# Optimization experiments

Hardware: AMD Instinct MI355X
Metric: run time of the kernel (lower is better)

The kernel has to match this reference:

```python
import math
import jax, jax.numpy as jnp
import numpy as np

N_HEAD = 16
N_GROUPS = 32
EPS = 1e-05


def gelu(x):
    return 0.5 * x * (1.0 + jnp.tanh(math.sqrt(2.0 / math.pi) * (x + 0.044715 * x ** 3)))


def dp_group_norm(x, weight, bias, num_groups=N_GROUPS, eps=EPS):
    # x: [B, T, H]. torch F.group_norm on transposed [B, H, T] normalizes over
    # (channels_per_group, T) jointly per (batch, group).
    B, T, H = x.shape
    xg = x.reshape(B, T, num_groups, H // num_groups)
    mean = jnp.mean(xg, axis=(1, 3), keepdims=True)
    var = jnp.mean((xg - mean) ** 2, axis=(1, 3), keepdims=True)
    xn = ((xg - mean) / jnp.sqrt(var + eps)).reshape(B, T, H)
    return xn * weight + bias


def attention(x, w_attn, b_attn, w_aproj, b_aproj):
    B, T, H = x.shape
    hd = H // N_HEAD
    qkv = x @ w_attn + b_attn                      # [B, T, 3H]
    q, k, v = jnp.split(qkv, 3, axis=-1)
    q = q.reshape(B, T, N_HEAD, hd).transpose(0, 2, 1, 3)   # [B, nh, T, hd]
    k = k.reshape(B, T, N_HEAD, hd).transpose(0, 2, 1, 3)   # [B, nh, T, hd]
    v = v.reshape(B, T, N_HEAD, hd).transpose(0, 2, 1, 3)
    w = jnp.einsum('bhqd,bhkd->bhqk', q, k)        # no 1/sqrt(d): scale=False
    causal = jnp.tril(jnp.ones((T, T), dtype=x.dtype))
    w = w * causal - 1e10 * (1.0 - causal)
    w = jax.nn.softmax(w, axis=-1)
    a = jnp.einsum('bhqk,bhkd->bhqd', w, v)        # [B, nh, T, hd]
    a = a.transpose(0, 2, 1, 3).reshape(B, T, H)
    a = a @ w_aproj + b_aproj
    present = jnp.stack((k, v))                    # [2, B, nh, T, hd]
    return a, present


def setup_inputs() -> dict:
    key = jax.random.key(0)
    ks = jax.random.split(key, 6)
    B, T, H = 2, 2048, 1024
    return {
        'x': jax.random.normal(ks[0], (B, T, H), dtype=jnp.float32),
        'w_attn': jax.random.normal(ks[1], (H, 3 * H), dtype=jnp.float32) * 0.02,
        'b_attn': jnp.zeros((3 * H,), dtype=jnp.float32),
        'w_aproj': jax.random.normal(ks[2], (H, H), dtype=jnp.float32) * 0.02,
        'b_aproj': jnp.zeros((H,), dtype=jnp.float32),
        'ln1_w': jnp.ones((H,), dtype=jnp.float32),
        'ln1_b': jnp.zeros((H,), dtype=jnp.float32),
        'ln2_w': jnp.ones((H,), dtype=jnp.float32),
        'ln2_b': jnp.zeros((H,), dtype=jnp.float32),
        'w_fc': jax.random.normal(ks[3], (H, 4 * H), dtype=jnp.float32) * 0.02,
        'b_fc': jnp.zeros((4 * H,), dtype=jnp.float32),
        'w_mproj': jax.random.normal(ks[4], (4 * H, H), dtype=jnp.float32) * 0.02,
        'b_mproj': jnp.zeros((H,), dtype=jnp.float32),
    }


def reference(x, w_attn, b_attn, w_aproj, b_aproj, ln1_w, ln1_b, ln2_w, ln2_b,
              w_fc, b_fc, w_mproj, b_mproj):
    a, present = attention(dp_group_norm(x, ln1_w, ln1_b), w_attn, b_attn, w_aproj, b_aproj)
    x = x + a
    h = gelu(dp_group_norm(x, ln2_w, ln2_b) @ w_fc + b_fc)
    m = h @ w_mproj + b_mproj
    x = x + m
    return (x, present)
```

## Files before the change

### kernel.cpp

```cpp
#include <hip/hip_runtime.h>

#define B_  2
#define T_  2048
#define H_  1024
#define NH_ 16
#define HD_ 64
#define M_  (B_*T_)
#define AS_ 72

typedef __bf16 bf16x8 __attribute__((ext_vector_type(8)));
typedef float  floatx4 __attribute__((ext_vector_type(4)));

typedef __attribute__((address_space(1))) const unsigned int gas_u32;
typedef __attribute__((address_space(3))) unsigned int       las_u32;

__device__ __forceinline__ void gload_lds16(const __bf16* g, __bf16* l) {
    __builtin_amdgcn_global_load_lds((gas_u32*)g, (las_u32*)l, 16, 0, 0);
}

__global__ __launch_bounds__(256) void transpose_bf16(
    const float* __restrict__ in, __bf16* __restrict__ out, int K, int N)
{
    __shared__ float tile[32][33];
    const int k0 = blockIdx.x * 32, n0 = blockIdx.y * 32;
    const int tx = threadIdx.x & 31, ty = threadIdx.x >> 5;
#pragma unroll
    for (int i = 0; i < 32; i += 8)
        tile[ty + i][tx] = in[(size_t)(k0 + ty + i) * N + (n0 + tx)];
    __syncthreads();
#pragma unroll
    for (int i = 0; i < 32; i += 8)
        out[(size_t)(n0 + ty + i) * K + (k0 + tx)] = (__bf16)tile[tx][ty + i];
}

__global__ __launch_bounds__(256) void gn_partial(
    const float* __restrict__ x, float2* __restrict__ part)
{
    const int bg = blockIdx.x, chunk = blockIdx.y;
    const int batch = bg >> 5, g = bg & 31;
    const float* xp = x + (size_t)batch * T_ * H_ + g * 32;
    float s = 0.f, ss = 0.f;
    for (int i = threadIdx.x; i < 128 * 32; i += 256) {
        const int t = chunk * 128 + (i >> 5), c = i & 31;
        const float v = xp[(size_t)t * H_ + c];
        s += v; ss += v * v;
    }
#pragma unroll
    for (int off = 32; off > 0; off >>= 1) {
        s  += __shfl_down(s,  off, 64);
        ss += __shfl_down(ss, off, 64);
    }
    __shared__ float rs[4], rss[4];
    const int wv = threadIdx.x >> 6, lane = threadIdx.x & 63;
    if (lane == 0) { rs[wv] = s; rss[wv] = ss; }
    __syncthreads();
    if (threadIdx.x == 0)
        part[bg * 16 + chunk] =
            make_float2(rs[0] + rs[1] + rs[2] + rs[3],
                        rss[0] + rss[1] + rss[2] + rss[3]);
}

__global__ __launch_bounds__(64) void gn_finalize(
    const float2* __restrict__ part, float2* __restrict__ stats)
{
    const int bg = threadIdx.x;
    float s = 0.f, ss = 0.f;
#pragma unroll
    for (int i = 0; i < 16; ++i) {
        const float2 p = part[bg * 16 + i];
        s += p.x; ss += p.y;
    }
    const float inv = 1.f / (float)(T_ * 32);
    const float mean = s * inv;
    const float var  = ss * inv - mean * mean;
    stats[bg] = make_float2(mean, rsqrtf(var + 1e-5f));
}

__global__ __launch_bounds__(256) void gn_apply(
    const float* __restrict__ x, const float2* __restrict__ stats,
    const float* __restrict__ w, const float* __restrict__ bsc,
    __bf16* __restrict__ out)
{
    const size_t idx = ((size_t)blockIdx.x * 256 + threadIdx.x) * 4;
    const int h = (int)(idx & (H_ - 1));
    const int batch = (int)(idx >> 21);
    const float2 mr = stats[batch * 32 + (h >> 5)];
    const float4 xv = *(const float4*)(x + idx);
    const float4 wv = *(const float4*)(w + h);
    const float4 bv = *(const float4*)(bsc + h);
    __bf16 o[4];
    o[0] = (__bf16)((xv.x - mr.x) * mr.y * wv.x + bv.x);
    o[1] = (__bf16)((xv.y - mr.x) * mr.y * wv.y + bv.y);
    o[2] = (__bf16)((xv.z - mr.x) * mr.y * wv.z + bv.z);
    o[3] = (__bf16)((xv.w - mr.x) * mr.y * wv.w + bv.w);
    *(uint2*)(out + idx) = *(uint2*)o;
}

__device__ __forceinline__ void gemm_core(
    const __bf16* __restrict__ A, const __bf16* __restrict__ BT,
    int K, int m0, int n0, __bf16* As, __bf16* Bs, floatx4 (&acc)[4][4])
{
    const int tid  = threadIdx.x;
    const int lane = tid & 63, wv = tid >> 6;
    const int quad = lane >> 4, l16 = lane & 15;
    const int wm = (wv >> 1) * 64, wn = (wv & 1) * 64;
    const int r0 = tid >> 2, cc0 = (tid & 3) * 8;

    const __bf16* Ag0 = A  + (size_t)(m0 + r0)      * K + cc0;
    const __bf16* Ag1 = A  + (size_t)(m0 + r0 + 64) * K + cc0;
    const __bf16* Bg0 = BT + (size_t)(n0 + r0)      * K + cc0;
    const __bf16* Bg1 = BT + (size_t)(n0 + r0 + 64) * K + cc0;
    __bf16* asd0 = As + tid * 8;
    __bf16* asd1 = As + 2048 + tid * 8;
    __bf16* bsd0 = Bs + tid * 8;
    __bf16* bsd1 = Bs + 2048 + tid * 8;

    for (int kt = 0; kt < K; kt += 32) {
        __syncthreads();
        gload_lds16(Ag0 + kt, asd0);
        gload_lds16(Ag1 + kt, asd1);
        gload_lds16(Bg0 + kt, bsd0);
        gload_lds16(Bg1 + kt, bsd1);
        __syncthreads();
        bf16x8 af[4], bfg[4];
#pragma unroll
        for (int i = 0; i < 4; ++i)
            af[i]  = *(const bf16x8*)(As + (wm + i * 16 + l16) * 32 + quad * 8);
#pragma unroll
        for (int i = 0; i < 4; ++i)
            bfg[i] = *(const bf16x8*)(Bs + (wn + i * 16 + l16) * 32 + quad * 8);
#pragma unroll
        for (int mi = 0; mi < 4; ++mi)
#pragma unroll
            for (int ni = 0; ni < 4; ++ni)
                acc[mi][ni] = __builtin_amdgcn_mfma_f32_16x16x32_bf16(
                    af[mi], bfg[ni], acc[mi][ni], 0, 0, 0);
    }
}

#define GEMM_PROLOGUE(KVAL)                                             \
    __shared__ __align__(16) __bf16 As[128 * 32], Bs[128 * 32];         \
    const int m0 = blockIdx.x * 128, n0 = blockIdx.y * 128;             \
    floatx4 acc[4][4];                                                  \
    { floatx4 z = {0.f, 0.f, 0.f, 0.f};                                 \
      for (int i = 0; i < 4; ++i) for (int j = 0; j < 4; ++j) acc[i][j] = z; } \
    gemm_core(A, BT, (KVAL), m0, n0, As, Bs, acc);                      \
    const int tid = threadIdx.x, lane = tid & 63, wv = tid >> 6;        \
    const int quad = lane >> 4, l16 = lane & 15;                        \
    const int wm = (wv >> 1) * 64, wn = (wv & 1) * 64;                  \
    (void)tid;

__global__ __launch_bounds__(256) void gemm_qkv(
    const __bf16* __restrict__ A, const __bf16* __restrict__ BT,
    const float* __restrict__ bias, __bf16* __restrict__ qb,
    __bf16* __restrict__ kb, __bf16* __restrict__ vtb,
    float* __restrict__ present)
{
    GEMM_PROLOGUE(H_)
#pragma unroll
    for (int ni = 0; ni < 4; ++ni) {
        const int col = n0 + wn + ni * 16 + l16;
        const float bv = bias[col];
        const int which = col >> 10, c = col & 1023, hh = c >> 6, d = c & 63;
#pragma unroll
        for (int mi = 0; mi < 4; ++mi)
#pragma unroll
            for (int r = 0; r < 4; ++r) {
                const int row = m0 + wm + mi * 16 + quad * 4 + r;
                const int bb = row >> 11, t = row & 2047;
                const float v = acc[mi][ni][r] + bv;
                const size_t idx = (((size_t)bb * NH_ + hh) * T_ + t) * HD_ + d;
                if (which == 0)      qb[idx] = (__bf16)v;
                else if (which == 1) { kb[idx] = (__bf16)v; present[idx] = v; }
                else { vtb[(((size_t)bb * NH_ + hh) * HD_ + d) * T_ + t] = (__bf16)v;
                       present[(size_t)B_ * NH_ * T_ * HD_ + idx] = v; }
            }
    }
}

__global__ __launch_bounds__(256) void gemm_gelu(
    const __bf16* __restrict__ A, const __bf16* __restrict__ BT,
    const float* __restrict__ bias, __bf16* __restrict__ out)
{
    GEMM_PROLOGUE(H_)
#pragma unroll
    for (int ni = 0; ni < 4; ++ni) {
        const int col = n0 + wn + ni * 16 + l16;
        const float bv = bias[col];
#pragma unroll
        for (int mi = 0; mi < 4; ++mi)
#pragma unroll
            for (int r = 0; r < 4; ++r) {
                const int row = m0 + wm + mi * 16 + quad * 4 + r;
                const float v = acc[mi][ni][r] + bv;
                const float g = 0.5f * v *
                    (1.f + tanhf(0.7978845608028654f * (v + 0.044715f * v * v * v)));
                out[(size_t)row * (4 * H_) + col] = (__bf16)g;
            }
    }
}

__global__ __launch_bounds__(256) void gemm_resid_n64(
    const __bf16* __restrict__ A, const __bf16* __restrict__ BT,
    const float* __restrict__ bias, const float* __restrict__ resid,
    float* __restrict__ out, int K, int N)
{
    __shared__ __align__(16) __bf16 As[128 * 32], Bs[64 * 32];
    const int m0 = blockIdx.x * 128, n0 = blockIdx.y * 64;
    const int tid  = threadIdx.x;
    const int lane = tid & 63, wv = tid >> 6;
    const int quad = lane >> 4, l16 = lane & 15;
    const int wm = (wv >> 1) * 64, wn = (wv & 1) * 32;
    const int r0 = tid >> 2, cc0 = (tid & 3) * 8;

    floatx4 acc[4][2];
    { floatx4 z = {0.f, 0.f, 0.f, 0.f};
#pragma unroll
      for (int i = 0; i < 4; ++i) { acc[i][0] = z; acc[i][1] = z; } }

    const __bf16* Ag0 = A  + (size_t)(m0 + r0)      * K + cc0;
    const __bf16* Ag1 = A  + (size_t)(m0 + r0 + 64) * K + cc0;
    const __bf16* Bg0 = BT + (size_t)(n0 + r0)      * K + cc0;
    __bf16* asd0 = As + tid * 8;
    __bf16* asd1 = As + 2048 + tid * 8;
    __bf16* bsd0 = Bs + tid * 8;

    for (int kt = 0; kt < K; kt += 32) {
        __syncthreads();
        gload_lds16(Ag0 + kt, asd0);
        gload_lds16(Ag1 + kt, asd1);
        gload_lds16(Bg0 + kt, bsd0);
        __syncthreads();
        bf16x8 af[4], bfg[2];
#pragma unroll
        for (int i = 0; i < 4; ++i)
            af[i]  = *(const bf16x8*)(As + (wm + i * 16 + l16) * 32 + quad * 8);
#pragma unroll
        for (int i = 0; i < 2; ++i)
            bfg[i] = *(const bf16x8*)(Bs + (wn + i * 16 + l16) * 32 + quad * 8);
#pragma unroll
        for (int mi = 0; mi < 4; ++mi)
#pragma unroll
            for (int ni = 0; ni < 2; ++ni)
                acc[mi][ni] = __builtin_amdgcn_mfma_f32_16x16x32_bf16(
                    af[mi], bfg[ni], acc[mi][ni], 0, 0, 0);
    }

#pragma unroll
    for (int ni = 0; ni < 2; ++ni) {
        const int col = n0 + wn + ni * 16 + l16;
        const float bv = bias[col];
#pragma unroll
        for (int mi = 0; mi < 4; ++mi)
#pragma unroll
            for (int r = 0; r < 4; ++r) {
                const int row = m0 + wm + mi * 16 + quad * 4 + r;
                const size_t idx = (size_t)row * N + col;
                out[idx] = acc[mi][ni][r] + bv + resid[idx];
            }
    }
}

__global__ __launch_bounds__(256) void attn_kernel(
    const __bf16* __restrict__ qb, const __bf16* __restrict__ kb,
    const __bf16* __restrict__ vtb, __bf16* __restrict__ aout)
{
    const int p = blockIdx.x, bh = blockIdx.y;
    const int bb = bh >> 4, hh = bh & 15;
    const __bf16* Q  = qb  + (size_t)bh * T_ * HD_;
    const __bf16* Kp = kb  + (size_t)bh * T_ * HD_;
    const __bf16* VT = vtb + (size_t)bh * HD_ * T_;
    __shared__ __align__(16) __bf16 Qs[128 * AS_], Ks[64 * AS_],
                                    Vts[64 * AS_], Ps[128 * AS_];

    const int tid = threadIdx.x, lane = tid & 63, wv = tid >> 6;
    const int quad = lane >> 4, l16 = lane & 15;
    const int r0 = tid >> 3, cc0 = (tid & 7) * 8;

    for (int half = 0; half < 2; ++half) {
        const int sp = half ? (15 - p) : p;
        const int q0 = sp * 128;
        const int nkt = 2 * sp + 2;

        __syncthreads();
#pragma unroll
        for (int c = tid; c < 1024; c += 256) {
            const int r = c >> 3, cc = (c & 7) * 8;
            *(uint4*)(Qs + r * AS_ + cc) =
                *(const uint4*)(Q + (size_t)(q0 + r) * HD_ + cc);
        }

        float m_i[2][4], l_i[2][4];
        floatx4 Ov[2][4];
        {
            floatx4 z = {0.f, 0.f, 0.f, 0.f};
#pragma unroll
            for (int mi = 0; mi < 2; ++mi)
#pragma unroll
                for (int i = 0; i < 4; ++i)
                    { Ov[mi][i] = z; m_i[mi][i] = -1e30f; l_i[mi][i] = 0.f; }
        }

        uint4 kr0, kr1, vr0, vr1;
        kr0 = *(const uint4*)(Kp + (size_t)(r0)      * HD_ + cc0);
        kr1 = *(const uint4*)(Kp + (size_t)(r0 + 32) * HD_ + cc0);
        vr0 = *(const uint4*)(VT + (size_t)(r0)      * T_ + cc0);
        vr1 = *(const uint4*)(VT + (size_t)(r0 + 32) * T_ + cc0);

        for (int kt = 0; kt < nkt; ++kt) {
            __syncthreads();
            *(uint4*)(Ks  + r0 * AS_ + cc0)        = kr0;
            *(uint4*)(Ks  + (r0 + 32) * AS_ + cc0) = kr1;
            *(uint4*)(Vts + r0 * AS_ + cc0)        = vr0;
            *(uint4*)(Vts + (r0 + 32) * AS_ + cc0) = vr1;
            __syncthreads();
            if (kt + 1 < nkt) {
                const int kn = kt + 1;
                kr0 = *(const uint4*)(Kp + (size_t)(kn * 64 + r0)      * HD_ + cc0);
                kr1 = *(const uint4*)(Kp + (size_t)(kn * 64 + r0 + 32) * HD_ + cc0);
                vr0 = *(const uint4*)(VT + (size_t)(r0)      * T_ + kn * 64 + cc0);
                vr1 = *(const uint4*)(VT + (size_t)(r0 + 32) * T_ + kn * 64 + cc0);
            }

            floatx4 sacc[2][4];
            { floatx4 z = {0.f, 0.f, 0.f, 0.f};
#pragma unroll
              for (int mi = 0; mi < 2; ++mi)
#pragma unroll
                  for (int i = 0; i < 4; ++i) sacc[mi][i] = z; }
#pragma unroll
            for (int kk = 0; kk < 2; ++kk) {
                bf16x8 aq[2];
#pragma unroll
                for (int mi = 0; mi < 2; ++mi)
                    aq[mi] = *(const bf16x8*)(Qs + (wv * 32 + mi * 16 + l16) * AS_ + kk * 32 + quad * 8);
#pragma unroll
                for (int ni = 0; ni < 4; ++ni) {
                    const bf16x8 bk = *(const bf16x8*)(Ks + (ni * 16 + l16) * AS_ + kk * 32 + quad * 8);
#pragma unroll
                    for (int mi = 0; mi < 2; ++mi)
                        sacc[mi][ni] = __builtin_amdgcn_mfma_f32_16x16x32_bf16(
                            aq[mi], bk, sacc[mi][ni], 0, 0, 0);
                }
            }
            if (kt >= 2 * sp) {
#pragma unroll
                for (int mi = 0; mi < 2; ++mi)
#pragma unroll
                    for (int ni = 0; ni < 4; ++ni) {
                        const int key = kt * 64 + ni * 16 + l16;
#pragma unroll
                        for (int r = 0; r < 4; ++r)
                            if (key > q0 + wv * 32 + mi * 16 + quad * 4 + r)
                                sacc[mi][ni][r] = -1e30f;
                    }
            }
#pragma unroll
            for (int mi = 0; mi < 2; ++mi) {
                float rmax[4], alpha[4], rsum[4];
#pragma unroll
                for (int r = 0; r < 4; ++r)
                    rmax[r] = fmaxf(fmaxf(sacc[mi][0][r], sacc[mi][1][r]),
                                    fmaxf(sacc[mi][2][r], sacc[mi][3][r]));
#pragma unroll
                for (int off = 1; off < 16; off <<= 1)
#pragma unroll
                    for (int r = 0; r < 4; ++r)
                        rmax[r] = fmaxf(rmax[r], __shfl_xor(rmax[r], off, 64));
#pragma unroll
                for (int r = 0; r < 4; ++r) {
                    const float mn = fmaxf(m_i[mi][r], rmax[r]);
                    alpha[r] = __expf(m_i[mi][r] - mn);
                    m_i[mi][r] = mn;
                    rsum[r] = 0.f;
                }
#pragma unroll
                for (int ni = 0; ni < 4; ++ni)
#pragma unroll
                    for (int r = 0; r < 4; ++r) {
                        const float pe = __expf(sacc[mi][ni][r] - m_i[mi][r]);
                        sacc[mi][ni][r] = pe;
                        rsum[r] += pe;
                    }
#pragma unroll
                for (int off = 1; off < 16; off <<= 1)
#pragma unroll
                    for (int r = 0; r < 4; ++r)
                        rsum[r] += __shfl_xor(rsum[r], off, 64);
#pragma unroll
                for (int r = 0; r < 4; ++r) {
                    l_i[mi][r] = l_i[mi][r] * alpha[r] + rsum[r];
#pragma unroll
                    for (int ni = 0; ni < 4; ++ni)
                        Ov[mi][ni][r] *= alpha[r];
                }
            }
#pragma unroll
            for (int mi = 0; mi < 2; ++mi)
#pragma unroll
                for (int ni = 0; ni < 4; ++ni)
#pragma unroll
                    for (int r = 0; r < 4; ++r)
                        Ps[(wv * 32 + mi * 16 + quad * 4 + r) * AS_ + ni * 16 + l16] =
                            (__bf16)sacc[mi][ni][r];
#pragma unroll
            for (int kk = 0; kk < 2; ++kk) {
                bf16x8 ap[2];
#pragma unroll
                for (int mi = 0; mi < 2; ++mi)
                    ap[mi] = *(const bf16x8*)(Ps + (wv * 32 + mi * 16 + l16) * AS_ + kk * 32 + quad * 8);
#pragma unroll
                for (int ni = 0; ni < 4; ++ni) {
                    const bf16x8 bv2 = *(const bf16x8*)(Vts + (ni * 16 + l16) * AS_ + kk * 32 + quad * 8);
#pragma unroll
                    for (int mi = 0; mi < 2; ++mi)
                        Ov[mi][ni] = __builtin_amdgcn_mfma_f32_16x16x32_bf16(
                            ap[mi], bv2, Ov[mi][ni], 0, 0, 0);
                }
            }
        }
#pragma unroll
        for (int mi = 0; mi < 2; ++mi)
#pragma unroll
            for (int ni = 0; ni < 4; ++ni)
#pragma unroll
                for (int r = 0; r < 4; ++r) {
                    const int t = q0 + wv * 32 + mi * 16 + quad * 4 + r;
                    aout[((size_t)(bb * T_ + t)) * H_ + hh * HD_ + ni * 16 + l16] =
                        (__bf16)(Ov[mi][ni][r] / l_i[mi][r]);
                }
    }
}

extern "C" void kernel_launch(void* const* d_in, const int* in_sizes, int n_in,
                              void* d_out, int out_size, void* d_ws, size_t ws_size,
                              hipStream_t stream)
{
    (void)in_sizes; (void)n_in; (void)out_size; (void)ws_size;
    const float* x       = (const float*)d_in[0];
    const float* w_attn  = (const float*)d_in[1];
    const float* b_attn  = (const float*)d_in[2];
    const float* w_aproj = (const float*)d_in[3];
    const float* b_aproj = (const float*)d_in[4];
    const float* ln1_w   = (const float*)d_in[5];
    const float* ln1_b   = (const float*)d_in[6];
    const float* ln2_w   = (const float*)d_in[7];
    const float* ln2_b   = (const float*)d_in[8];
    const float* w_fc    = (const float*)d_in[9];
    const float* b_fc    = (const float*)d_in[10];
    const float* w_mproj = (const float*)d_in[11];
    const float* b_mproj = (const float*)d_in[12];
    float* out = (float*)d_out;
    float* present = out + (size_t)M_ * H_;

    char* wp = (char*)d_ws;
    auto alloc = [&](size_t bytes) {
        void* p = (void*)wp; wp += (bytes + 255) & ~(size_t)255; return p;
    };
    __bf16* A1       = (__bf16*)alloc((size_t)M_ * H_ * 2);
    __bf16* A2       = (__bf16*)alloc((size_t)M_ * H_ * 2);
    __bf16* WattnT   = (__bf16*)alloc((size_t)3 * H_ * H_ * 2);
    __bf16* WaprojT  = (__bf16*)alloc((size_t)H_ * H_ * 2);
    __bf16* WfcT     = (__bf16*)alloc((size_t)4 * H_ * H_ * 2);
    __bf16* WmprojT  = (__bf16*)alloc((size_t)4 * H_ * H_ * 2);
    __bf16* qb       = (__bf16*)alloc((size_t)M_ * H_ * 2);
    __bf16* kb       = (__bf16*)alloc((size_t)M_ * H_ * 2);
    __bf16* vtb      = (__bf16*)alloc((size_t)M_ * H_ * 2);
    __bf16* attn_out = (__bf16*)alloc((size_t)M_ * H_ * 2);
    float*  x2       = (float*) alloc((size_t)M_ * H_ * 4);
    __bf16* Hbuf     = (__bf16*)alloc((size_t)M_ * 4 * H_ * 2);
    float2* gn_part  = (float2*)alloc(64 * 16 * sizeof(float2));
    float2* gn_stats = (float2*)alloc(64 * sizeof(float2));

    transpose_bf16<<<dim3(H_/32, 3*H_/32), 256, 0, stream>>>(w_attn,  WattnT,  H_,   3*H_);
    transpose_bf16<<<dim3(H_/32, H_/32),   256, 0, stream>>>(w_aproj, WaprojT, H_,   H_);
    transpose_bf16<<<dim3(H_/32, 4*H_/32), 256, 0, stream>>>(w_fc,    WfcT,    H_,   4*H_);
    transpose_bf16<<<dim3(4*H_/32, H_/32), 256, 0, stream>>>(w_mproj, WmprojT, 4*H_, H_);

    gn_partial <<<dim3(64, 16), 256, 0, stream>>>(x, gn_part);
    gn_finalize<<<1, 64, 0, stream>>>(gn_part, gn_stats);
    gn_apply   <<<M_*H_/1024, 256, 0, stream>>>(x, gn_stats, ln1_w, ln1_b, A1);

    gemm_qkv<<<dim3(M_/128, 3*H_/128), 256, 0, stream>>>(A1, WattnT, b_attn,
                                                         qb, kb, vtb, present);
    attn_kernel<<<dim3(8, B_*NH_), 256, 0, stream>>>(qb, kb, vtb, attn_out);
    gemm_resid_n64<<<dim3(M_/128, H_/64), 256, 0, stream>>>(attn_out, WaprojT, b_aproj,
                                                            x, x2, H_, H_);

    gn_partial <<<dim3(64, 16), 256, 0, stream>>>(x2, gn_part);
    gn_finalize<<<1, 64, 0, stream>>>(gn_part, gn_stats);
    gn_apply   <<<M_*H_/1024, 256, 0, stream>>>(x2, gn_stats, ln2_w, ln2_b, A2);

    gemm_gelu<<<dim3(M_/128, 4*H_/128), 256, 0, stream>>>(A2, WfcT, b_fc, Hbuf);
    gemm_resid_n64<<<dim3(M_/128, H_/64), 256, 0, stream>>>(Hbuf, WmprojT, b_mproj,
                                                            x2, out, 4*H_, H_);
}
```

Baseline: 462.9 us.

## Double GEMM K-step per barrier and retile attention to 64-row query blocks

```diff
diff --git a/kernel.cpp b/kernel.cpp
--- a/kernel.cpp
+++ b/kernel.cpp
@@ -6,7 +6,7 @@
 #define NH_ 16
 #define HD_ 64
 #define M_  (B_*T_)
-#define AS_ 72
+#define PS_ 72
 
 typedef __bf16 bf16x8 __attribute__((ext_vector_type(8)));
 typedef float  floatx4 __attribute__((ext_vector_type(4)));
@@ -104,42 +104,42 @@
     const int lane = tid & 63, wv = tid >> 6;
     const int quad = lane >> 4, l16 = lane & 15;
     const int wm = (wv >> 1) * 64, wn = (wv & 1) * 64;
-    const int r0 = tid >> 2, cc0 = (tid & 3) * 8;
-
-    const __bf16* Ag0 = A  + (size_t)(m0 + r0)      * K + cc0;
-    const __bf16* Ag1 = A  + (size_t)(m0 + r0 + 64) * K + cc0;
-    const __bf16* Bg0 = BT + (size_t)(n0 + r0)      * K + cc0;
-    const __bf16* Bg1 = BT + (size_t)(n0 + r0 + 64) * K + cc0;
-    __bf16* asd0 = As + tid * 8;
-    __bf16* asd1 = As + 2048 + tid * 8;
-    __bf16* bsd0 = Bs + tid * 8;
-    __bf16* bsd1 = Bs + 2048 + tid * 8;
-
-    for (int kt = 0; kt < K; kt += 32) {
+    const int r0 = tid >> 2, c0 = (tid & 3) * 8;
+
+    const __bf16* Ag = A  + (size_t)(m0 + r0) * K + c0;
+    const __bf16* Bg = BT + (size_t)(n0 + r0) * K + c0;
+
+    for (int kt = 0; kt < K; kt += 64) {
         __syncthreads();
-        gload_lds16(Ag0 + kt, asd0);
-        gload_lds16(Ag1 + kt, asd1);
-        gload_lds16(Bg0 + kt, bsd0);
-        gload_lds16(Bg1 + kt, bsd1);
+#pragma unroll
+        for (int s = 0; s < 2; ++s) {
+            gload_lds16(Ag + kt + s * 32,                As + s * 4096 + tid * 8);
+            gload_lds16(Ag + (size_t)64 * K + kt + s * 32, As + s * 4096 + 2048 + tid * 8);
+            gload_lds16(Bg + kt + s * 32,                Bs + s * 4096 + tid * 8);
+            gload_lds16(Bg + (size_t)64 * K + kt + s * 32, Bs + s * 4096 + 2048 + tid * 8);
+        }
         __syncthreads();
-        bf16x8 af[4], bfg[4];
-#pragma unroll
-        for (int i = 0; i < 4; ++i)
-            af[i]  = *(const bf16x8*)(As + (wm + i * 16 + l16) * 32 + quad * 8);
-#pragma unroll
-        for (int i = 0; i < 4; ++i)
-            bfg[i] = *(const bf16x8*)(Bs + (wn + i * 16 + l16) * 32 + quad * 8);
-#pragma unroll
-        for (int mi = 0; mi < 4; ++mi)
-#pragma unroll
-            for (int ni = 0; ni < 4; ++ni)
-                acc[mi][ni] = __builtin_amdgcn_mfma_f32_16x16x32_bf16(
-                    af[mi], bfg[ni], acc[mi][ni], 0, 0, 0);
+#pragma unroll
+        for (int kk = 0; kk < 2; ++kk) {
+            bf16x8 af[4], bfg[4];
+#pragma unroll
+            for (int i = 0; i < 4; ++i)
+                af[i]  = *(const bf16x8*)(As + kk * 4096 + (wm + i * 16 + l16) * 32 + quad * 8);
+#pragma unroll
+            for (int i = 0; i < 4; ++i)
+                bfg[i] = *(const bf16x8*)(Bs + kk * 4096 + (wn + i * 16 + l16) * 32 + quad * 8);
+#pragma unroll
+            for (int mi = 0; mi < 4; ++mi)
+#pragma unroll
+                for (int ni = 0; ni < 4; ++ni)
+                    acc[mi][ni] = __builtin_amdgcn_mfma_f32_16x16x32_bf16(
+                        af[mi], bfg[ni], acc[mi][ni], 0, 0, 0);
+        }
     }
 }
 
 #define GEMM_PROLOGUE(KVAL)                                             \
-    __shared__ __align__(16) __bf16 As[128 * 32], Bs[128 * 32];         \
+    __shared__ __align__(16) __bf16 As[2 * 4096], Bs[2 * 4096];         \
     const int m0 = blockIdx.x * 128, n0 = blockIdx.y * 128;             \
     floatx4 acc[4][4];                                                  \
     { floatx4 z = {0.f, 0.f, 0.f, 0.f};                                 \
@@ -205,45 +205,47 @@
     const float* __restrict__ bias, const float* __restrict__ resid,
     float* __restrict__ out, int K, int N)
 {
-    __shared__ __align__(16) __bf16 As[128 * 32], Bs[64 * 32];
+    __shared__ __align__(16) __bf16 As[2 * 4096], Bs[2 * 2048];
     const int m0 = blockIdx.x * 128, n0 = blockIdx.y * 64;
     const int tid  = threadIdx.x;
     const int lane = tid & 63, wv = tid >> 6;
     const int quad = lane >> 4, l16 = lane & 15;
     const int wm = (wv >> 1) * 64, wn = (wv & 1) * 32;
-    const int r0 = tid >> 2, cc0 = (tid & 3) * 8;
+    const int r0 = tid >> 2, c0 = (tid & 3) * 8;
 
     floatx4 acc[4][2];
     { floatx4 z = {0.f, 0.f, 0.f, 0.f};
 #pragma unroll
       for (int i = 0; i < 4; ++i) { acc[i][0] = z; acc[i][1] = z; } }
 
-    const __bf16* Ag0 = A  + (size_t)(m0 + r0)      * K + cc0;
-    const __bf16* Ag1 = A  + (size_t)(m0 + r0 + 64) * K + cc0;
-    const __bf16* Bg0 = BT + (size_t)(n0 + r0)      * K + cc0;
-    __bf16* asd0 = As + tid * 8;
-    __bf16* asd1 = As + 2048 + tid * 8;
-    __bf16* bsd0 = Bs + tid * 8;
-
-    for (int kt = 0; kt < K; kt += 32) {
+    const __bf16* Ag = A  + (size_t)(m0 + r0) * K + c0;
+    const __bf16* Bg = BT + (size_t)(n0 + r0) * K + c0;
+
+    for (int kt = 0; kt < K; kt += 64) {
         __syncthreads();
-        gload_lds16(Ag0 + kt, asd0);
-        gload_lds16(Ag1 + kt, asd1);
-        gload_lds16(Bg0 + kt, bsd0);
+#pragma unroll
+        for (int s = 0; s < 2; ++s) {
+            gload_lds16(Ag + kt + s * 32,                  As + s * 4096 + tid * 8);
+            gload_lds16(Ag + (size_t)64 * K + kt + s * 32, As + s * 4096 + 2048 + tid * 8);
+            gload_lds16(Bg + kt + s * 32,                  Bs + s * 2048 + tid * 8);
+        }
         __syncthreads();
-        bf16x8 af[4], bfg[2];
-#pragma unroll
-        for (int i = 0; i < 4; ++i)
-            af[i]  = *(const bf16x8*)(As + (wm + i * 16 + l16) * 32 + quad * 8);
-#pragma unroll
-        for (int i = 0; i < 2; ++i)
-            bfg[i] = *(const bf16x8*)(Bs + (wn + i * 16 + l16) * 32 + quad * 8);
-#pragma unroll
-        for (int mi = 0; mi < 4; ++mi)
-#pragma unroll
-            for (int ni = 0; ni < 2; ++ni)
-                acc[mi][ni] = __builtin_amdgcn_mfma_f32_16x16x32_bf16(
-                    af[mi], bfg[ni], acc[mi][ni], 0, 0, 0);
+#pragma unroll
+        for (int kk = 0; kk < 2; ++kk) {
+            bf16x8 af[4], bfg[2];
+#pragma unroll
+            for (int i = 0; i < 4; ++i)
+                af[i]  = *(const bf16x8*)(As + kk * 4096 + (wm + i * 16 + l16) * 32 + quad * 8);
+#pragma unroll
+            for (int i = 0; i < 2; ++i)
+                bfg[i] = *(const bf16x8*)(Bs + kk * 2048 + (wn + i * 16 + l16) * 32 + quad * 8);
+#pragma unroll
+            for (int mi = 0; mi < 4; ++mi)
+#pragma unroll
+                for (int ni = 0; ni < 2; ++ni)
+                    acc[mi][ni] = __builtin_amdgcn_mfma_f32_16x16x32_bf16(
+                        af[mi], bfg[ni], acc[mi][ni], 0, 0, 0);
+        }
     }
 
 #pragma unroll
@@ -265,170 +267,131 @@
     const __bf16* __restrict__ qb, const __bf16* __restrict__ kb,
     const __bf16* __restrict__ vtb, __bf16* __restrict__ aout)
 {
-    const int p = blockIdx.x, bh = blockIdx.y;
+    const int bh = blockIdx.x, pr = blockIdx.y;
     const int bb = bh >> 4, hh = bh & 15;
     const __bf16* Q  = qb  + (size_t)bh * T_ * HD_;
     const __bf16* Kp = kb  + (size_t)bh * T_ * HD_;
     const __bf16* VT = vtb + (size_t)bh * HD_ * T_;
-    __shared__ __align__(16) __bf16 Qs[128 * AS_], Ks[64 * AS_],
-                                    Vts[64 * AS_], Ps[128 * AS_];
+    __shared__ __align__(16) __bf16 Qs[2 * 2048], Ks[2 * 2048], Vs[2 * 2048];
+    __shared__ __align__(16) __bf16 Ps[64 * PS_];
 
     const int tid = threadIdx.x, lane = tid & 63, wv = tid >> 6;
     const int quad = lane >> 4, l16 = lane & 15;
-    const int r0 = tid >> 3, cc0 = (tid & 7) * 8;
+    const int sr = tid >> 2, sc = (tid & 3) * 8;
 
     for (int half = 0; half < 2; ++half) {
-        const int sp = half ? (15 - p) : p;
-        const int q0 = sp * 128;
-        const int nkt = 2 * sp + 2;
+        const int sp = half ? (31 - pr) : pr;
+        const int q0 = sp * 64;
+        const int nkt = sp + 1;
 
         __syncthreads();
 #pragma unroll
-        for (int c = tid; c < 1024; c += 256) {
-            const int r = c >> 3, cc = (c & 7) * 8;
-            *(uint4*)(Qs + r * AS_ + cc) =
-                *(const uint4*)(Q + (size_t)(q0 + r) * HD_ + cc);
-        }
-
-        float m_i[2][4], l_i[2][4];
-        floatx4 Ov[2][4];
-        {
-            floatx4 z = {0.f, 0.f, 0.f, 0.f};
-#pragma unroll
-            for (int mi = 0; mi < 2; ++mi)
-#pragma unroll
-                for (int i = 0; i < 4; ++i)
-                    { Ov[mi][i] = z; m_i[mi][i] = -1e30f; l_i[mi][i] = 0.f; }
-        }
-
-        uint4 kr0, kr1, vr0, vr1;
-        kr0 = *(const uint4*)(Kp + (size_t)(r0)      * HD_ + cc0);
-        kr1 = *(const uint4*)(Kp + (size_t)(r0 + 32) * HD_ + cc0);
-        vr0 = *(const uint4*)(VT + (size_t)(r0)      * T_ + cc0);
-        vr1 = *(const uint4*)(VT + (size_t)(r0 + 32) * T_ + cc0);
+        for (int s = 0; s < 2; ++s) {
+            gload_lds16(Q  + (size_t)(q0 + sr) * HD_ + s * 32 + sc, Qs + s * 2048 + tid * 8);
+            gload_lds16(Kp + (size_t)sr * HD_ + s * 32 + sc,        Ks + s * 2048 + tid * 8);
+            gload_lds16(VT + (size_t)sr * T_  + s * 32 + sc,        Vs + s * 2048 + tid * 8);
+        }
+
+        float m_i[4], l_i[4];
+        floatx4 Ov[4];
+        { floatx4 z = {0.f, 0.f, 0.f, 0.f};
+#pragma unroll
+          for (int i = 0; i < 4; ++i) { Ov[i] = z; m_i[i] = -1e30f; l_i[i] = 0.f; } }
 
         for (int kt = 0; kt < nkt; ++kt) {
             __syncthreads();
-            *(uint4*)(Ks  + r0 * AS_ + cc0)        = kr0;
-            *(uint4*)(Ks  + (r0 + 32) * AS_ + cc0) = kr1;
-            *(uint4*)(Vts + r0 * AS_ + cc0)        = vr0;
-            *(uint4*)(Vts + (r0 + 32) * AS_ + cc0) = vr1;
+
+            floatx4 sacc[4];
+            { floatx4 z = {0.f, 0.f, 0.f, 0.f};
+#pragma unroll
+              for (int i = 0; i < 4; ++i) sacc[i] = z; }
+#pragma unroll
+            for (int kk = 0; kk < 2; ++kk) {
+                const bf16x8 aq = *(const bf16x8*)(Qs + kk * 2048 + (wv * 16 + l16) * 32 + quad * 8);
+#pragma unroll
+                for (int ni = 0; ni < 4; ++ni) {
+                    const bf16x8 bk = *(const bf16x8*)(Ks + kk * 2048 + (ni * 16 + l16) * 32 + quad * 8);
+                    sacc[ni] = __builtin_amdgcn_mfma_f32_16x16x32_bf16(aq, bk, sacc[ni], 0, 0, 0);
+                }
+            }
+            if (kt == sp) {
+#pragma unroll
+                for (int ni = 0; ni < 4; ++ni) {
+                    const int keyL = ni * 16 + l16;
+#pragma unroll
+                    for (int r = 0; r < 4; ++r)
+                        if (keyL > quad * 4 + r + wv * 16) sacc[ni][r] = -1e30f;
+                }
+            }
+            float rmax[4], alpha[4], rsum[4];
+#pragma unroll
+            for (int r = 0; r < 4; ++r)
+                rmax[r] = fmaxf(fmaxf(sacc[0][r], sacc[1][r]),
+                                fmaxf(sacc[2][r], sacc[3][r]));
+#pragma unroll
+            for (int off = 1; off < 16; off <<= 1)
+#pragma unroll
+                for (int r = 0; r < 4; ++r)
+                    rmax[r] = fmaxf(rmax[r], __shfl_xor(rmax[r], off, 64));
+#pragma unroll
+            for (int r = 0; r < 4; ++r) {
+                const float mn = fmaxf(m_i[r], rmax[r]);
+                alpha[r] = __expf(m_i[r] - mn);
+                m_i[r] = mn;
+                rsum[r] = 0.f;
+            }
+#pragma unroll
+            for (int ni = 0; ni < 4; ++ni)
+#pragma unroll
+                for (int r = 0; r < 4; ++r) {
+                    const float pe = __expf(sacc[ni][r] - m_i[r]);
+                    sacc[ni][r] = pe;
+                    rsum[r] += pe;
+                }
+#pragma unroll
+            for (int off = 1; off < 16; off <<= 1)
+#pragma unroll
+                for (int r = 0; r < 4; ++r)
+                    rsum[r] += __shfl_xor(rsum[r], off, 64);
+#pragma unroll
+            for (int r = 0; r < 4; ++r) {
+                l_i[r] = l_i[r] * alpha[r] + rsum[r];
+#pragma unroll
+                for (int ni = 0; ni < 4; ++ni)
+                    Ov[ni][r] *= alpha[r];
+            }
+#pragma unroll
+            for (int ni = 0; ni < 4; ++ni)
+#pragma unroll
+                for (int r = 0; r < 4; ++r)
+                    Ps[(wv * 16 + quad * 4 + r) * PS_ + ni * 16 + l16] = (__bf16)sacc[ni][r];
+#pragma unroll
+            for (int kk = 0; kk < 2; ++kk) {
+                const bf16x8 ap = *(const bf16x8*)(Ps + (wv * 16 + l16) * PS_ + kk * 32 + quad * 8);
+#pragma unroll
+                for (int ni = 0; ni < 4; ++ni) {
+                    const bf16x8 bv2 = *(const bf16x8*)(Vs + kk * 2048 + (ni * 16 + l16) * 32 + quad * 8);
+                    Ov[ni] = __builtin_amdgcn_mfma_f32_16x16x32_bf16(ap, bv2, Ov[ni], 0, 0, 0);
+                }
+            }
             __syncthreads();
             if (kt + 1 < nkt) {
                 const int kn = kt + 1;
-                kr0 = *(const uint4*)(Kp + (size_t)(kn * 64 + r0)      * HD_ + cc0);
-                kr1 = *(const uint4*)(Kp + (size_t)(kn * 64 + r0 + 32) * HD_ + cc0);
-                vr0 = *(const uint4*)(VT + (size_t)(r0)      * T_ + kn * 64 + cc0);
-                vr1 = *(const uint4*)(VT + (size_t)(r0 + 32) * T_ + kn * 64 + cc0);
-            }
-
-            floatx4 sacc[2][4];
-            { floatx4 z = {0.f, 0.f, 0.f, 0.f};
-#pragma unroll
-              for (int mi = 0; mi < 2; ++mi)
-#pragma unroll
-                  for (int i = 0; i < 4; ++i) sacc[mi][i] = z; }
-#pragma unroll
-            for (int kk = 0; kk < 2; ++kk) {
-                bf16x8 aq[2];
-#pragma unroll
-                for (int mi = 0; mi < 2; ++mi)
-                    aq[mi] = *(const bf16x8*)(Qs + (wv * 32 + mi * 16 + l16) * AS_ + kk * 32 + quad * 8);
-#pragma unroll
-                for (int ni = 0; ni < 4; ++ni) {
-                    const bf16x8 bk = *(const bf16x8*)(Ks + (ni * 16 + l16) * AS_ + kk * 32 + quad * 8);
-#pragma unroll
-                    for (int mi = 0; mi < 2; ++mi)
-                        sacc[mi][ni] = __builtin_amdgcn_mfma_f32_16x16x32_bf16(
-                            aq[mi], bk, sacc[mi][ni], 0, 0, 0);
+#pragma unroll
+                for (int s = 0; s < 2; ++s) {
+                    gload_lds16(Kp + (size_t)(kn * 64 + sr) * HD_ + s * 32 + sc, Ks + s * 2048 + tid * 8);
+                    gload_lds16(VT + (size_t)sr * T_ + kn * 64 + s * 32 + sc,    Vs + s * 2048 + tid * 8);
                 }
             }
-            if (kt >= 2 * sp) {
-#pragma unroll
-                for (int mi = 0; mi < 2; ++mi)
-#pragma unroll
-                    for (int ni = 0; ni < 4; ++ni) {
-                        const int key = kt * 64 + ni * 16 + l16;
-#pragma unroll
-                        for (int r = 0; r < 4; ++r)
-                            if (key > q0 + wv * 32 + mi * 16 + quad * 4 + r)
-                                sacc[mi][ni][r] = -1e30f;
-                    }
-            }
-#pragma unroll
-            for (int mi = 0; mi < 2; ++mi) {
-                float rmax[4], alpha[4], rsum[4];
-#pragma unroll
-                for (int r = 0; r < 4; ++r)
-                    rmax[r] = fmaxf(fmaxf(sacc[mi][0][r], sacc[mi][1][r]),
-                                    fmaxf(sacc[mi][2][r], sacc[mi][3][r]));
-#pragma unroll
-                for (int off = 1; off < 16; off <<= 1)
-#pragma unroll
-                    for (int r = 0; r < 4; ++r)
-                        rmax[r] = fmaxf(rmax[r], __shfl_xor(rmax[r], off, 64));
-#pragma unroll
-                for (int r = 0; r < 4; ++r) {
-                    const float mn = fmaxf(m_i[mi][r], rmax[r]);
-                    alpha[r] = __expf(m_i[mi][r] - mn);
-                    m_i[mi][r] = mn;
-                    rsum[r] = 0.f;
-                }
-#pragma unroll
-                for (int ni = 0; ni < 4; ++ni)
-#pragma unroll
-                    for (int r = 0; r < 4; ++r) {
-                        const float pe = __expf(sacc[mi][ni][r] - m_i[mi][r]);
-                        sacc[mi][ni][r] = pe;
-                        rsum[r] += pe;
-                    }
-#pragma unroll
-                for (int off = 1; off < 16; off <<= 1)
-#pragma unroll
-                    for (int r = 0; r < 4; ++r)
-                        rsum[r] += __shfl_xor(rsum[r], off, 64);
-#pragma unroll
-                for (int r = 0; r < 4; ++r) {
-                    l_i[mi][r] = l_i[mi][r] * alpha[r] + rsum[r];
-#pragma unroll
-                    for (int ni = 0; ni < 4; ++ni)
-                        Ov[mi][ni][r] *= alpha[r];
-                }
-            }
-#pragma unroll
-            for (int mi = 0; mi < 2; ++mi)
-#pragma unroll
-                for (int ni = 0; ni < 4; ++ni)
-#pragma unroll
-                    for (int r = 0; r < 4; ++r)
-                        Ps[(wv * 32 + mi * 16 + quad * 4 + r) * AS_ + ni * 16 + l16] =
-                            (__bf16)sacc[mi][ni][r];
-#pragma unroll
-            for (int kk = 0; kk < 2; ++kk) {
-                bf16x8 ap[2];
-#pragma unroll
-                for (int mi = 0; mi < 2; ++mi)
-                    ap[mi] = *(const bf16x8*)(Ps + (wv * 32 + mi * 16 + l16) * AS_ + kk * 32 + quad * 8);
-#pragma unroll
-                for (int ni = 0; ni < 4; ++ni) {
-                    const bf16x8 bv2 = *(const bf16x8*)(Vts + (ni * 16 + l16) * AS_ + kk * 32 + quad * 8);
-#pragma unroll
-                    for (int mi = 0; mi < 2; ++mi)
-                        Ov[mi][ni] = __builtin_amdgcn_mfma_f32_16x16x32_bf16(
-                            ap[mi], bv2, Ov[mi][ni], 0, 0, 0);
-                }
-            }
-        }
-#pragma unroll
-        for (int mi = 0; mi < 2; ++mi)
-#pragma unroll
-            for (int ni = 0; ni < 4; ++ni)
-#pragma unroll
-                for (int r = 0; r < 4; ++r) {
-                    const int t = q0 + wv * 32 + mi * 16 + quad * 4 + r;
-                    aout[((size_t)(bb * T_ + t)) * H_ + hh * HD_ + ni * 16 + l16] =
-                        (__bf16)(Ov[mi][ni][r] / l_i[mi][r]);
-                }
+        }
+#pragma unroll
+        for (int ni = 0; ni < 4; ++ni)
+#pragma unroll
+            for (int r = 0; r < 4; ++r) {
+                const int t = q0 + wv * 16 + quad * 4 + r;
+                aout[((size_t)(bb * T_ + t)) * H_ + hh * HD_ + ni * 16 + l16] =
+                    (__bf16)(Ov[ni][r] / l_i[r]);
+            }
     }
 }
 
@@ -483,7 +446,7 @@
 
     gemm_qkv<<<dim3(M_/128, 3*H_/128), 256, 0, stream>>>(A1, WattnT, b_attn,
                                                          qb, kb, vtb, present);
-    attn_kernel<<<dim3(8, B_*NH_), 256, 0, stream>>>(qb, kb, vtb, attn_out);
+    attn_kernel<<<dim3(32, 16), 256, 0, stream>>>(qb, kb, vtb, attn_out);
     gemm_resid_n64<<<dim3(M_/128, H_/64), 256, 0, stream>>>(attn_out, WaprojT, b_aproj,
                                                             x, x2, H_, H_);
 
```

Result: faster. 432.6 us (-6.5%).
